# Optimization experiments

Measured on AMD Instinct MI355X. Metric: run time of the kernel, lower is better.

The kernel has to match this reference:

```python
import jax, jax.numpy as jnp
import numpy as np

B, NQ, NK, D = 64, 1024, 1024, 128
MASK_VALUE = -1e6


def setup_inputs() -> dict:
    key = jax.random.key(0)
    kq, kk, kv, kl = jax.random.split(key, 4)
    queries = jax.random.normal(kq, (B, NQ, D), dtype=jnp.float32)
    keys = jax.random.normal(kk, (B, NK, D), dtype=jnp.float32)
    values = jax.random.normal(kv, (B, NK, D), dtype=jnp.float32)
    valid_lens = jax.random.randint(kl, (B,), 1, NK + 1, dtype=jnp.int32)
    return {"queries": queries, "keys": keys, "values": values, "valid_lens": valid_lens}


def reference(queries, keys, values, valid_lens):
    d = queries.shape[-1]
    # scores: [B, Nq, Nk]
    scores = jnp.einsum("bqd,bkd->bqk", queries, keys) / jnp.sqrt(jnp.float32(d))
    # valid_lens [B] -> mask over last (key) axis, same for every query row
    key_pos = jnp.arange(scores.shape[-1])  # [Nk]
    mask = key_pos[None, None, :] < valid_lens[:, None, None]  # [B,1,Nk] broadcast
    scores = jnp.where(mask, scores, jnp.float32(MASK_VALUE))
    attn = jax.nn.softmax(scores, axis=-1)
    # dropout p=0.0 (eval): identity
    return jnp.einsum("bqk,bkd->bqd", attn, values)
```

## Files before the change

### kernel.cpp

```cpp
#include <hip/hip_runtime.h>

typedef __bf16 bf16x8 __attribute__((ext_vector_type(8)));
typedef __bf16 bf16x4 __attribute__((ext_vector_type(4)));
typedef __bf16 bf16x2 __attribute__((ext_vector_type(2)));
typedef float f32x4 __attribute__((ext_vector_type(4)));
typedef int i32x4 __attribute__((ext_vector_type(4)));

namespace {
constexpr int kNQ = 1024;
constexpr int kNK = 1024;
constexpr int kD = 128;
constexpr int kBQ = 64;
constexpr int kBK = 32;
constexpr int kKStride = 136;
constexpr int kVStride = 32;
constexpr float kScaleLog2e = 0.12751742f;
}

__device__ __forceinline__ int packbf(float a, float b) {
    bf16x2 t; t[0] = (__bf16)a; t[1] = (__bf16)b;
    return __builtin_bit_cast(int, t);
}

__global__ void lpt_sort(const int* __restrict__ VL, int* __restrict__ perm) {
    const int t = threadIdx.x;
    const int v = VL[t];
    int rank = 0;
    for (int j = 0; j < 64; ++j) {
        const int vj = VL[j];
        rank += (vj > v) || (vj == v && j < t);
    }
    perm[rank] = t;
}

__global__ __launch_bounds__(256, 4)
void fa_fwd(const float* __restrict__ Q, const float* __restrict__ K,
            const float* __restrict__ V, const int* __restrict__ VL,
            const int* __restrict__ perm, float* __restrict__ O)
{
    __shared__ __align__(16) __bf16 kls[2][kBK * kKStride];
    __shared__ __align__(16) __bf16 vls[2][kD * kVStride];

    const int tid  = threadIdx.x;
    const int wave = tid >> 6;
    const int lane = tid & 63;
    const int quad = lane >> 4;
    const int c16  = lane & 15;

    const int b    = perm[blockIdx.x >> 4];
    const int qblk = blockIdx.x & 15;
    const int q0   = qblk * kBQ + wave * 16;

    const int valid  = VL[b];
    const int ntiles = (valid + kBK - 1) / kBK;

    bf16x8 qf[4];
    {
        const float* qp = Q + ((size_t)b * kNQ + q0 + c16) * kD + quad * 8;
        #pragma unroll
        for (int f = 0; f < 4; ++f) {
            #pragma unroll
            for (int j = 0; j < 8; ++j) qf[f][j] = (__bf16)qp[f * 32 + j];
        }
    }

    bf16x8 ones;
    #pragma unroll
    for (int j = 0; j < 8; ++j) ones[j] = (__bf16)1.0f;

    f32x4 acc[9];
    #pragma unroll
    for (int f = 0; f < 9; ++f) {
        acc[f][0] = 0.f; acc[f][1] = 0.f; acc[f][2] = 0.f; acc[f][3] = 0.f;
    }

    const int ksrow = tid >> 3;
    const int kscol = (tid & 7) * 16;
    const int vkg   = (tid & 7) * 4;
    const int vdb   = (tid >> 3) * 4;

    f32x4 kr[4], vr[4];

    auto load_regs = [&](int kbase) {
        const float* kp = K + ((size_t)b * kNK + kbase + ksrow) * kD + kscol;
        #pragma unroll
        for (int i = 0; i < 4; ++i) kr[i] = *(const f32x4*)(kp + i * 4);
        const float* vp = V + ((size_t)b * kNK + kbase + vkg) * kD + vdb;
        #pragma unroll
        for (int i = 0; i < 4; ++i) vr[i] = *(const f32x4*)(vp + (size_t)i * kD);
    };

    auto cvt_write = [&](int bufi) {
        bf16x8 kh;
        #pragma unroll
        for (int j = 0; j < 8; ++j) kh[j] = (__bf16)kr[j >> 2][j & 3];
        *(bf16x8*)&kls[bufi][ksrow * kKStride + kscol] = kh;
        #pragma unroll
        for (int j = 0; j < 8; ++j) kh[j] = (__bf16)kr[2 + (j >> 2)][j & 3];
        *(bf16x8*)&kls[bufi][ksrow * kKStride + kscol + 8] = kh;
        #pragma unroll
        for (int j = 0; j < 4; ++j) {
            bf16x4 vh;
            #pragma unroll
            for (int i = 0; i < 4; ++i) vh[i] = (__bf16)vr[i][j];
            *(bf16x4*)&vls[bufi][(vdb + j) * kVStride + vkg] = vh;
        }
    };

    const int a0 = ((quad & 1) << 7) + (c16 << 2);
    const int a1 = a0 + 64;

    load_regs(0);
    cvt_write(0);
    __syncthreads();

    int cur = 0;
    for (int t = 0; t < ntiles; ++t) {
        const int kb = t * kBK;
        const bool more = (t + 1 < ntiles);
        if (more) load_regs(kb + kBK);

        f32x4 s0a = {0.f,0.f,0.f,0.f}, s0b = {0.f,0.f,0.f,0.f};
        f32x4 s1a = {0.f,0.f,0.f,0.f}, s1b = {0.f,0.f,0.f,0.f};
        const __bf16* kbuf = kls[cur];
        #pragma unroll
        for (int f = 0; f < 2; ++f) {
            bf16x8 kf = *(const bf16x8*)&kbuf[c16 * kKStride + f * 32 + quad * 8];
            s0a = __builtin_amdgcn_mfma_f32_16x16x32_bf16(kf, qf[f], s0a, 0, 0, 0);
        }
        #pragma unroll
        for (int f = 2; f < 4; ++f) {
            bf16x8 kf = *(const bf16x8*)&kbuf[c16 * kKStride + f * 32 + quad * 8];
            s0b = __builtin_amdgcn_mfma_f32_16x16x32_bf16(kf, qf[f], s0b, 0, 0, 0);
        }
        #pragma unroll
        for (int f = 0; f < 2; ++f) {
            bf16x8 kf = *(const bf16x8*)&kbuf[(16 + c16) * kKStride + f * 32 + quad * 8];
            s1a = __builtin_amdgcn_mfma_f32_16x16x32_bf16(kf, qf[f], s1a, 0, 0, 0);
        }
        #pragma unroll
        for (int f = 2; f < 4; ++f) {
            bf16x8 kf = *(const bf16x8*)&kbuf[(16 + c16) * kKStride + f * 32 + quad * 8];
            s1b = __builtin_amdgcn_mfma_f32_16x16x32_bf16(kf, qf[f], s1b, 0, 0, 0);
        }
        f32x4 s0 = s0a + s0b;
        f32x4 s1 = s1a + s1b;

        if (kb + kBK > valid) {
            #pragma unroll
            for (int r = 0; r < 4; ++r) {
                if (kb + quad * 4 + r >= valid)      s0[r] = -1e30f;
                if (kb + 16 + quad * 4 + r >= valid) s1[r] = -1e30f;
            }
        }

        #pragma unroll
        for (int r = 0; r < 4; ++r) {
            s0[r] = exp2f(s0[r] * kScaleLog2e);
            s1[r] = exp2f(s1[r] * kScaleLog2e);
        }

        const int pp01 = packbf(s0[0], s0[1]), pp23 = packbf(s0[2], s0[3]);
        const int qq01 = packbf(s1[0], s1[1]), qq23 = packbf(s1[2], s1[3]);
        const int b0p = __builtin_amdgcn_ds_bpermute(a0, pp01);
        const int b0q = __builtin_amdgcn_ds_bpermute(a0, qq01);
        const int b1p = __builtin_amdgcn_ds_bpermute(a0, pp23);
        const int b1q = __builtin_amdgcn_ds_bpermute(a0, qq23);
        const int b2p = __builtin_amdgcn_ds_bpermute(a1, pp01);
        const int b2q = __builtin_amdgcn_ds_bpermute(a1, qq01);
        const int b3p = __builtin_amdgcn_ds_bpermute(a1, pp23);
        const int b3q = __builtin_amdgcn_ds_bpermute(a1, qq23);
        const bool lo = quad < 2;
        i32x4 pd;
        pd[0] = lo ? b0p : b0q;
        pd[1] = lo ? b1p : b1q;
        pd[2] = lo ? b2p : b2q;
        pd[3] = lo ? b3p : b3q;
        const bf16x8 pf = __builtin_bit_cast(bf16x8, pd);

        if (more) cvt_write(cur ^ 1);

        const __bf16* vbuf = vls[cur];
        #pragma unroll
        for (int f = 0; f < 8; ++f) {
            const bf16x8 vf = *(const bf16x8*)&vbuf[(f * 16 + c16) * kVStride + quad * 8];
            acc[f] = __builtin_amdgcn_mfma_f32_16x16x32_bf16(pf, vf, acc[f], 0, 0, 0);
        }
        acc[8] = __builtin_amdgcn_mfma_f32_16x16x32_bf16(pf, ones, acc[8], 0, 0, 0);

        __syncthreads();
        cur ^= 1;
    }

    float* ob = O + ((size_t)b * kNQ + q0) * kD;
    #pragma unroll
    for (int r = 0; r < 4; ++r) {
        const float inv = 1.0f / acc[8][r];
        #pragma unroll
        for (int f = 0; f < 8; ++f) {
            ob[(quad * 4 + r) * kD + f * 16 + c16] = acc[f][r] * inv;
        }
    }
}

extern "C" void kernel_launch(void* const* d_in, const int* in_sizes, int n_in,
                              void* d_out, int out_size, void* d_ws, size_t ws_size,
                              hipStream_t stream) {
    const float* Q = (const float*)d_in[0];
    const float* K = (const float*)d_in[1];
    const float* V = (const float*)d_in[2];
    const int*  VL = (const int*)d_in[3];
    float* O = (float*)d_out;
    int* perm = (int*)d_ws;
    lpt_sort<<<1, 64, 0, stream>>>(VL, perm);
    fa_fwd<<<dim3(64 * 16), 256, 0, stream>>>(Q, K, V, VL, perm, O);
}
```

Measured before the change: 183.9 us.

## Use persistent blocks with an atomic work queue sorted by tile count

Replaces the one-block-per-item launch with a persistent grid of 768 blocks. Each block pulls (batch, q-block) items from a queue sorted in descending order of key-tile count, using an atomic counter. The queue-building kernel now ranks all 1024 items, not 64 batches. This aims to even out load across CUs when valid lengths vary. In exchange it adds an atomic and a barrier per item, and 1024 threads each run a 1024-step rank loop.

Result: slower. 252.7 us (+37.4%).

```diff
diff --git a/kernel.cpp b/kernel.cpp
--- a/kernel.cpp
+++ b/kernel.cpp
@@ -14,6 +14,8 @@
 constexpr int kBK = 32;
 constexpr int kKStride = 136;
 constexpr int kVStride = 32;
+constexpr int kNItems = 1024;
+constexpr int kGrid = 768;
 constexpr float kScaleLog2e = 0.12751742f;
 }
 
@@ -22,24 +24,29 @@
     return __builtin_bit_cast(int, t);
 }
 
-__global__ void lpt_sort(const int* __restrict__ VL, int* __restrict__ perm) {
-    const int t = threadIdx.x;
-    const int v = VL[t];
+__global__ void build_queue(const int* __restrict__ VL, int* __restrict__ ws) {
+    __shared__ int svl[64];
+    const int tid = threadIdx.x;
+    if (tid < 64) svl[tid] = VL[tid];
+    __syncthreads();
+    const int mykey = (svl[tid >> 4] + 31) >> 5;
     int rank = 0;
-    for (int j = 0; j < 64; ++j) {
-        const int vj = VL[j];
-        rank += (vj > v) || (vj == v && j < t);
+    for (int j = 0; j < kNItems; ++j) {
+        const int kj = (svl[j >> 4] + 31) >> 5;
+        rank += (kj > mykey) || (kj == mykey && j < tid);
     }
-    perm[rank] = t;
+    ws[16 + rank] = tid;
+    if (tid == 0) ws[0] = kGrid;
 }
 
 __global__ __launch_bounds__(256, 4)
 void fa_fwd(const float* __restrict__ Q, const float* __restrict__ K,
             const float* __restrict__ V, const int* __restrict__ VL,
-            const int* __restrict__ perm, float* __restrict__ O)
+            int* __restrict__ ws, float* __restrict__ O)
 {
     __shared__ __align__(16) __bf16 kls[2][kBK * kKStride];
     __shared__ __align__(16) __bf16 vls[2][kD * kVStride];
+    __shared__ int next_s;
 
     const int tid  = threadIdx.x;
     const int wave = tid >> 6;
@@ -47,159 +54,168 @@
     const int quad = lane >> 4;
     const int c16  = lane & 15;
 
-    const int b    = perm[blockIdx.x >> 4];
-    const int qblk = blockIdx.x & 15;
-    const int q0   = qblk * kBQ + wave * 16;
-
-    const int valid  = VL[b];
-    const int ntiles = (valid + kBK - 1) / kBK;
-
-    bf16x8 qf[4];
-    {
-        const float* qp = Q + ((size_t)b * kNQ + q0 + c16) * kD + quad * 8;
-        #pragma unroll
-        for (int f = 0; f < 4; ++f) {
-            #pragma unroll
-            for (int j = 0; j < 8; ++j) qf[f][j] = (__bf16)qp[f * 32 + j];
-        }
-    }
+    const int* itemlist = ws + 16;
 
     bf16x8 ones;
     #pragma unroll
     for (int j = 0; j < 8; ++j) ones[j] = (__bf16)1.0f;
-
-    f32x4 acc[9];
-    #pragma unroll
-    for (int f = 0; f < 9; ++f) {
-        acc[f][0] = 0.f; acc[f][1] = 0.f; acc[f][2] = 0.f; acc[f][3] = 0.f;
-    }
 
     const int ksrow = tid >> 3;
     const int kscol = (tid & 7) * 16;
     const int vkg   = (tid & 7) * 4;
     const int vdb   = (tid >> 3) * 4;
 
-    f32x4 kr[4], vr[4];
-
-    auto load_regs = [&](int kbase) {
-        const float* kp = K + ((size_t)b * kNK + kbase + ksrow) * kD + kscol;
-        #pragma unroll
-        for (int i = 0; i < 4; ++i) kr[i] = *(const f32x4*)(kp + i * 4);
-        const float* vp = V + ((size_t)b * kNK + kbase + vkg) * kD + vdb;
-        #pragma unroll
-        for (int i = 0; i < 4; ++i) vr[i] = *(const f32x4*)(vp + (size_t)i * kD);
-    };
-
-    auto cvt_write = [&](int bufi) {
-        bf16x8 kh;
-        #pragma unroll
-        for (int j = 0; j < 8; ++j) kh[j] = (__bf16)kr[j >> 2][j & 3];
-        *(bf16x8*)&kls[bufi][ksrow * kKStride + kscol] = kh;
-        #pragma unroll
-        for (int j = 0; j < 8; ++j) kh[j] = (__bf16)kr[2 + (j >> 2)][j & 3];
-        *(bf16x8*)&kls[bufi][ksrow * kKStride + kscol + 8] = kh;
-        #pragma unroll
-        for (int j = 0; j < 4; ++j) {
-            bf16x4 vh;
-            #pragma unroll
-            for (int i = 0; i < 4; ++i) vh[i] = (__bf16)vr[i][j];
-            *(bf16x4*)&vls[bufi][(vdb + j) * kVStride + vkg] = vh;
-        }
-    };
-
     const int a0 = ((quad & 1) << 7) + (c16 << 2);
     const int a1 = a0 + 64;
 
-    load_regs(0);
-    cvt_write(0);
-    __syncthreads();
-
-    int cur = 0;
-    for (int t = 0; t < ntiles; ++t) {
-        const int kb = t * kBK;
-        const bool more = (t + 1 < ntiles);
-        if (more) load_regs(kb + kBK);
-
-        f32x4 s0a = {0.f,0.f,0.f,0.f}, s0b = {0.f,0.f,0.f,0.f};
-        f32x4 s1a = {0.f,0.f,0.f,0.f}, s1b = {0.f,0.f,0.f,0.f};
-        const __bf16* kbuf = kls[cur];
+    f32x4 kr[4], vr[4];
+
+    for (int item = blockIdx.x; item < kNItems; ) {
+        const int code = itemlist[item];
+        const int b    = code >> 4;
+        const int qblk = code & 15;
+        const int q0   = qblk * kBQ + wave * 16;
+
+        const int valid  = VL[b];
+        const int ntiles = (valid + kBK - 1) / kBK;
+
+        bf16x8 qf[4];
+        {
+            const float* qp = Q + ((size_t)b * kNQ + q0 + c16) * kD + quad * 8;
+            #pragma unroll
+            for (int f = 0; f < 4; ++f) {
+                #pragma unroll
+                for (int j = 0; j < 8; ++j) qf[f][j] = (__bf16)qp[f * 32 + j];
+            }
+        }
+
+        f32x4 acc[9];
         #pragma unroll
-        for (int f = 0; f < 2; ++f) {
-            bf16x8 kf = *(const bf16x8*)&kbuf[c16 * kKStride + f * 32 + quad * 8];
-            s0a = __builtin_amdgcn_mfma_f32_16x16x32_bf16(kf, qf[f], s0a, 0, 0, 0);
-        }
-        #pragma unroll
-        for (int f = 2; f < 4; ++f) {
-            bf16x8 kf = *(const bf16x8*)&kbuf[c16 * kKStride + f * 32 + quad * 8];
-            s0b = __builtin_amdgcn_mfma_f32_16x16x32_bf16(kf, qf[f], s0b, 0, 0, 0);
-        }
-        #pragma unroll
-        for (int f = 0; f < 2; ++f) {
-            bf16x8 kf = *(const bf16x8*)&kbuf[(16 + c16) * kKStride + f * 32 + quad * 8];
-            s1a = __builtin_amdgcn_mfma_f32_16x16x32_bf16(kf, qf[f], s1a, 0, 0, 0);
-        }
-        #pragma unroll
-        for (int f = 2; f < 4; ++f) {
-            bf16x8 kf = *(const bf16x8*)&kbuf[(16 + c16) * kKStride + f * 32 + quad * 8];
-            s1b = __builtin_amdgcn_mfma_f32_16x16x32_bf16(kf, qf[f], s1b, 0, 0, 0);
-        }
-        f32x4 s0 = s0a + s0b;
-        f32x4 s1 = s1a + s1b;
-
-        if (kb + kBK > valid) {
+        for (int f = 0; f < 9; ++f) {
+            acc[f][0] = 0.f; acc[f][1] = 0.f; acc[f][2] = 0.f; acc[f][3] = 0.f;
+        }
+
+        auto load_regs = [&](int kbase) {
+            const float* kp = K + ((size_t)b * kNK + kbase + ksrow) * kD + kscol;
+            #pragma unroll
+            for (int i = 0; i < 4; ++i) kr[i] = *(const f32x4*)(kp + i * 4);
+            const float* vp = V + ((size_t)b * kNK + kbase + vkg) * kD + vdb;
+            #pragma unroll
+            for (int i = 0; i < 4; ++i) vr[i] = *(const f32x4*)(vp + (size_t)i * kD);
+        };
+
+        auto cvt_write = [&](int bufi) {
+            bf16x8 kh;
+            #pragma unroll
+            for (int j = 0; j < 8; ++j) kh[j] = (__bf16)kr[j >> 2][j & 3];
+            *(bf16x8*)&kls[bufi][ksrow * kKStride + kscol] = kh;
+            #pragma unroll
+            for (int j = 0; j < 8; ++j) kh[j] = (__bf16)kr[2 + (j >> 2)][j & 3];
+            *(bf16x8*)&kls[bufi][ksrow * kKStride + kscol + 8] = kh;
+            #pragma unroll
+            for (int j = 0; j < 4; ++j) {
+                bf16x4 vh;
+                #pragma unroll
+                for (int i = 0; i < 4; ++i) vh[i] = (__bf16)vr[i][j];
+                *(bf16x4*)&vls[bufi][(vdb + j) * kVStride + vkg] = vh;
+            }
+        };
+
+        load_regs(0);
+        cvt_write(0);
+        __syncthreads();
+
+        int cur = 0;
+        for (int t = 0; t < ntiles; ++t) {
+            const int kb = t * kBK;
+            const bool more = (t + 1 < ntiles);
+            if (more) load_regs(kb + kBK);
+
+            f32x4 s0a = {0.f,0.f,0.f,0.f}, s0b = {0.f,0.f,0.f,0.f};
+            f32x4 s1a = {0.f,0.f,0.f,0.f}, s1b = {0.f,0.f,0.f,0.f};
+            const __bf16* kbuf = kls[cur];
+            #pragma unroll
+            for (int f = 0; f < 2; ++f) {
+                bf16x8 kf = *(const bf16x8*)&kbuf[c16 * kKStride + f * 32 + quad * 8];
+                s0a = __builtin_amdgcn_mfma_f32_16x16x32_bf16(kf, qf[f], s0a, 0, 0, 0);
+            }
+            #pragma unroll
+            for (int f = 2; f < 4; ++f) {
+                bf16x8 kf = *(const bf16x8*)&kbuf[c16 * kKStride + f * 32 + quad * 8];
+                s0b = __builtin_amdgcn_mfma_f32_16x16x32_bf16(kf, qf[f], s0b, 0, 0, 0);
+            }
+            #pragma unroll
+            for (int f = 0; f < 2; ++f) {
+                bf16x8 kf = *(const bf16x8*)&kbuf[(16 + c16) * kKStride + f * 32 + quad * 8];
+                s1a = __builtin_amdgcn_mfma_f32_16x16x32_bf16(kf, qf[f], s1a, 0, 0, 0);
+            }
+            #pragma unroll
+            for (int f = 2; f < 4; ++f) {
+                bf16x8 kf = *(const bf16x8*)&kbuf[(16 + c16) * kKStride + f * 32 + quad * 8];
+                s1b = __builtin_amdgcn_mfma_f32_16x16x32_bf16(kf, qf[f], s1b, 0, 0, 0);
+            }
+            f32x4 s0 = s0a + s0b;
+            f32x4 s1 = s1a + s1b;
+
+            if (kb + kBK > valid) {
+                #pragma unroll
+                for (int r = 0; r < 4; ++r) {
+                    if (kb + quad * 4 + r >= valid)      s0[r] = -1e30f;
+                    if (kb + 16 + quad * 4 + r >= valid) s1[r] = -1e30f;
+                }
+            }
+
             #pragma unroll
             for (int r = 0; r < 4; ++r) {
-                if (kb + quad * 4 + r >= valid)      s0[r] = -1e30f;
-                if (kb + 16 + quad * 4 + r >= valid) s1[r] = -1e30f;
-            }
-        }
-
+                s0[r] = exp2f(s0[r] * kScaleLog2e);
+                s1[r] = exp2f(s1[r] * kScaleLog2e);
+            }
+
+            const int pp01 = packbf(s0[0], s0[1]), pp23 = packbf(s0[2], s0[3]);
+            const int qq01 = packbf(s1[0], s1[1]), qq23 = packbf(s1[2], s1[3]);
+            const int b0p = __builtin_amdgcn_ds_bpermute(a0, pp01);
+            const int b0q = __builtin_amdgcn_ds_bpermute(a0, qq01);
+            const int b1p = __builtin_amdgcn_ds_bpermute(a0, pp23);
+            const int b1q = __builtin_amdgcn_ds_bpermute(a0, qq23);
+            const int b2p = __builtin_amdgcn_ds_bpermute(a1, pp01);
+            const int b2q = __builtin_amdgcn_ds_bpermute(a1, qq01);
+            const int b3p = __builtin_amdgcn_ds_bpermute(a1, pp23);
+            const int b3q = __builtin_amdgcn_ds_bpermute(a1, qq23);
+            const bool lo = quad < 2;
+            i32x4 pd;
+            pd[0] = lo ? b0p : b0q;
+            pd[1] = lo ? b1p : b1q;
+            pd[2] = lo ? b2p : b2q;
+            pd[3] = lo ? b3p : b3q;
+            const bf16x8 pf = __builtin_bit_cast(bf16x8, pd);
+
+            if (more) cvt_write(cur ^ 1);
+
+            const __bf16* vbuf = vls[cur];
+            #pragma unroll
+            for (int f = 0; f < 8; ++f) {
+                const bf16x8 vf = *(const bf16x8*)&vbuf[(f * 16 + c16) * kVStride + quad * 8];
+                acc[f] = __builtin_amdgcn_mfma_f32_16x16x32_bf16(pf, vf, acc[f], 0, 0, 0);
+            }
+            acc[8] = __builtin_amdgcn_mfma_f32_16x16x32_bf16(pf, ones, acc[8], 0, 0, 0);
+
+            __syncthreads();
+            cur ^= 1;
+        }
+
+        float* ob = O + ((size_t)b * kNQ + q0) * kD;
         #pragma unroll
         for (int r = 0; r < 4; ++r) {
-            s0[r] = exp2f(s0[r] * kScaleLog2e);
-            s1[r] = exp2f(s1[r] * kScaleLog2e);
-        }
-
-        const int pp01 = packbf(s0[0], s0[1]), pp23 = packbf(s0[2], s0[3]);
-        const int qq01 = packbf(s1[0], s1[1]), qq23 = packbf(s1[2], s1[3]);
-        const int b0p = __builtin_amdgcn_ds_bpermute(a0, pp01);
-        const int b0q = __builtin_amdgcn_ds_bpermute(a0, qq01);
-        const int b1p = __builtin_amdgcn_ds_bpermute(a0, pp23);
-        const int b1q = __builtin_amdgcn_ds_bpermute(a0, qq23);
-        const int b2p = __builtin_amdgcn_ds_bpermute(a1, pp01);
-        const int b2q = __builtin_amdgcn_ds_bpermute(a1, qq01);
-        const int b3p = __builtin_amdgcn_ds_bpermute(a1, pp23);
-        const int b3q = __builtin_amdgcn_ds_bpermute(a1, qq23);
-        const bool lo = quad < 2;
-        i32x4 pd;
-        pd[0] = lo ? b0p : b0q;
-        pd[1] = lo ? b1p : b1q;
-        pd[2] = lo ? b2p : b2q;
-        pd[3] = lo ? b3p : b3q;
-        const bf16x8 pf = __builtin_bit_cast(bf16x8, pd);
-
-        if (more) cvt_write(cur ^ 1);
-
-        const __bf16* vbuf = vls[cur];
-        #pragma unroll
-        for (int f = 0; f < 8; ++f) {
-            const bf16x8 vf = *(const bf16x8*)&vbuf[(f * 16 + c16) * kVStride + quad * 8];
-            acc[f] = __builtin_amdgcn_mfma_f32_16x16x32_bf16(pf, vf, acc[f], 0, 0, 0);
-        }
-        acc[8] = __builtin_amdgcn_mfma_f32_16x16x32_bf16(pf, ones, acc[8], 0, 0, 0);
-
+            const float inv = 1.0f / acc[8][r];
+            #pragma unroll
+            for (int f = 0; f < 8; ++f) {
+                ob[(quad * 4 + r) * kD + f * 16 + c16] = acc[f][r] * inv;
+            }
+        }
+
+        if (tid == 0) next_s = atomicAdd(&ws[0], 1);
         __syncthreads();
-        cur ^= 1;
-    }
-
-    float* ob = O + ((size_t)b * kNQ + q0) * kD;
-    #pragma unroll
-    for (int r = 0; r < 4; ++r) {
-        const float inv = 1.0f / acc[8][r];
-        #pragma unroll
-        for (int f = 0; f < 8; ++f) {
-            ob[(quad * 4 + r) * kD + f * 16 + c16] = acc[f][r] * inv;
-        }
+        item = next_s;
     }
 }
 
@@ -211,7 +227,7 @@
     const float* V = (const float*)d_in[2];
     const int*  VL = (const int*)d_in[3];
     float* O = (float*)d_out;
-    int* perm = (int*)d_ws;
-    lpt_sort<<<1, 64, 0, stream>>>(VL, perm);
-    fa_fwd<<<dim3(64 * 16), 256, 0, stream>>>(Q, K, V, VL, perm, O);
-}
+    int* ws = (int*)d_ws;
+    build_queue<<<1, 1024, 0, stream>>>(VL, ws);
+    fa_fwd<<<dim3(kGrid), 256, 0, stream>>>(Q, K, V, VL, ws, O);
+}
```
